# Optimization experiments

Measured on AMD Instinct MI355X. Metric: run time of the kernel, lower is better.

Reference implementation:

```python
import jax, jax.numpy as jnp
import numpy as np

LS = (0, 1, 2)
DIMS = tuple(2 * l + 1 for l in LS)          # (1, 3, 5)
MULS = (128, 64, 32)                          # node irreps multiplicities (= attention*heads)
ATT_MULS = (16, 8, 4)                         # attention_irreps multiplicities per head
N_HEADS = 8
N_IRREPS_ATT = sum(ATT_MULS)                  # 28
ATTN_NORM = 1.0 / np.sqrt(N_IRREPS_ATT)
CG = tuple(1.0 / np.sqrt(d) for d in DIMS)    # l (x) l -> 0e Clebsch-Gordan coefficient
N_NODES = 512
EDGE_ATTR_DIM = 32
NODE_DIM = sum(m * d for m, d in zip(MULS, DIMS))  # 480


def split_irreps(x, muls):
    """Split last axis into per-l blocks [..., mul_l, 2l+1]."""
    out, i = [], 0
    for mul, d in zip(muls, DIMS):
        out.append(x[..., i:i + mul * d].reshape(x.shape[:-1] + (mul, d)))
        i += mul * d
    return out


def merge_irreps(parts):
    return jnp.concatenate([p.reshape(p.shape[:-2] + (-1,)) for p in parts], axis=-1)


def e3_linear(parts, Ws):
    # equivariant linear: mixes multiplicities within each l, 1/sqrt(mul_in) norm
    return [jnp.einsum('nim,io->nom', p, W) / np.sqrt(p.shape[-2])
            for p, W in zip(parts, Ws)]


def setup_inputs() -> dict:
    key = jax.random.key(0)
    ks = jax.random.split(key, 16)
    inp = {
        'node_feat': jax.random.normal(ks[0], (N_NODES, NODE_DIM), jnp.float32),
        'edge_attr': jax.random.normal(ks[1], (N_NODES, N_NODES, EDGE_ATTR_DIM), jnp.float32),
        'edge_sh':   jax.random.normal(ks[2], (N_NODES, N_NODES, sum(DIMS)), jnp.float32),
    }
    i = 3
    for nm in ('Wq', 'Wk', 'Wv'):
        for l, mul in enumerate(MULS):
            inp[f'{nm}{l}'] = jax.random.normal(ks[i], (mul, mul), jnp.float32)
            i += 1
    inp['mW1'] = jax.random.normal(ks[i], (EDGE_ATTR_DIM + 2 * sum(MULS), 64), jnp.float32) * 0.05
    inp['mb1'] = jnp.zeros((64,), jnp.float32)
    inp['mW2'] = jax.random.normal(ks[i + 1], (64, 64), jnp.float32) * 0.1
    inp['mb2'] = jnp.zeros((64,), jnp.float32)
    inp['mW3'] = jax.random.normal(ks[i + 2], (64, N_HEADS), jnp.float32) * 0.1
    inp['mb3'] = jnp.zeros((N_HEADS,), jnp.float32)
    return inp


def reference(node_feat, edge_attr, edge_sh,
              Wq0, Wq1, Wq2, Wk0, Wk1, Wk2, Wv0, Wv1, Wv2,
              mW1, mb1, mW2, mb2, mW3, mb3):
    N = node_feat.shape[0]
    nf = split_irreps(node_feat, MULS)                 # per-l: [N, mul_l, 2l+1]
    sh = split_irreps(edge_sh, (1, 1, 1))              # per-l: [N, N, 1, 2l+1]

    def to_heads(parts):
        return [p.reshape(N, N_HEADS, am, d) for p, am, d in zip(parts, ATT_MULS, DIMS)]

    q = to_heads(e3_linear(nf, (Wq0, Wq1, Wq2)))
    k = to_heads(e3_linear(nf, (Wk0, Wk1, Wk2)))
    v = to_heads(e3_linear(nf, (Wv0, Wv1, Wv2)))

    # node (x) edge_sh -> scalars (0e): same-l inner products, CG = 1/sqrt(2l+1)
    feat_rec = jnp.concatenate(
        [jnp.einsum('rim,rsm->rsi', p, s[..., 0, :]) * c for p, s, c in zip(nf, sh, CG)], axis=-1)
    feat_snd = jnp.concatenate(
        [jnp.einsum('sim,rsm->rsi', p, s[..., 0, :]) * c for p, s, c in zip(nf, sh, CG)], axis=-1)
    edge_feat = jnp.concatenate([edge_attr, feat_rec, feat_snd], axis=-1)  # [N,N,480]

    h = jnp.tanh(edge_feat @ mW1 + mb1)
    h = jnp.tanh(h @ mW2 + mb2)
    edge_weight = h @ mW3 + mb3                        # [N, N, H]

    # elementwise q (x) k -> 0e, summed over irreps (== scaled dot product per head)
    logits = sum(jnp.einsum('rhim,shim->rsh', qp, kp) * c
                 for qp, kp, c in zip(q, k, CG))       # [N, N, H]
    weight = jax.nn.softmax(logits * ATTN_NORM + edge_weight, axis=-2)  # softmax over senders

    # weighted aggregation over senders, per irrep
    upd = [jnp.einsum('rsh,shim->rhim', weight, vp) for vp in v]
    # axis_to_mul: [N, H, mul, d] -> [N, H*mul, d]
    upd = [u.reshape(N, N_HEADS * am, d) for u, am, d in zip(upd, ATT_MULS, DIMS)]

    return node_feat + merge_irreps(upd)               # residual (irreps match)
```

## Files before the change

kernel.cpp:

```cpp
#include <hip/hip_runtime.h>
#include <hip/hip_bf16.h>
#include <stdint.h>


#define NNODES 512
#define NDIM   480

#define QG_OFF    0u
#define W2B_OFF   131072u
#define W3B_OFF   133120u
#define KG_OFF    245760u
#define VB_OFF    491520u
#define ARE_OFF   737280u
#define ASN_OFF   884736u
#define WF_OFF    1032192u
#define FLAG_OFF  1040384u
#define L_OFF     1040448u
#define WTQ_OFF   3137600u
#define WTK_OFF   3159104u
#define WTV_OFF   3180608u
#define W1T_OFF   3202112u

typedef float f32x4 __attribute__((ext_vector_type(4)));
typedef short s16x8 __attribute__((ext_vector_type(8)));

__device__ __forceinline__ float bf2f(uint16_t u) {
    return __uint_as_float(((uint32_t)u) << 16);
}
__device__ __forceinline__ uint16_t f2bf(float f) {
    union { __hip_bfloat16 h; uint16_t u; } cv;
    cv.h = __float2bfloat16(f);
    return cv.u;
}
__device__ __forceinline__ uint32_t packbf(float lo, float hi) {
    return ((uint32_t)f2bf(hi) << 16) | (uint32_t)f2bf(lo);
}
__device__ __forceinline__ float ldin(const void* p, size_t i, int f32) {
    return f32 ? ((const float*)p)[i] : bf2f(((const uint16_t*)p)[i]);
}
__device__ __forceinline__ float ftanh(float x) {
    float e = __builtin_amdgcn_exp2f(x * 2.885390081777927f);
    return 1.0f - 2.0f * __builtin_amdgcn_rcpf(e + 1.0f);
}

#define NS 16384
__global__ __launch_bounds__(256) void kW(
    const void* __restrict__ mW1, const void* __restrict__ mb1,
    const void* __restrict__ mW2, const void* __restrict__ mb2,
    const void* __restrict__ mW3, const void* __restrict__ mb3,
    const void* __restrict__ Wq0, const void* __restrict__ Wq1, const void* __restrict__ Wq2,
    const void* __restrict__ Wk0, const void* __restrict__ Wk1, const void* __restrict__ Wk2,
    const void* __restrict__ Wv0, const void* __restrict__ Wv1, const void* __restrict__ Wv2,
    float* __restrict__ ws, const void* __restrict__ nfu, int* __restrict__ flagp)
{
    __shared__ int sflag;
    const int t = threadIdx.x;
    if (t < 64) {
        uint32_t x = ((const uint32_t*)nfu)[64 + t];
        int e = (x >> 7) & 0xff;
        int good = (x != 0u) && (e >= 100) && (e <= 140);
        unsigned long long m = __ballot(good);
        if (t == 0) sflag = (__popcll(m) < 32) ? 1 : 0;
    }
    __syncthreads();
    const int f32 = sflag;
    if (blockIdx.x == 0 && t == 0) flagp[0] = f32;

    const int gt = blockIdx.x * 256 + t;
    float* Wf = ws + WF_OFF;

    for (int i = gt; i < 2048; i += NS) Wf[i] = ldin(mW1, i, f32);
    for (int i = gt; i < 64; i += NS) Wf[6656 + i] = ldin(mb1, i, f32);
    for (int i = gt; i < 64; i += NS) Wf[6720 + i] = ldin(mb2, i, f32);
    for (int i = gt; i < 8; i += NS)  Wf[6784 + i] = ldin(mb3, i, f32);

    {
        uint32_t* W2B = (uint32_t*)(ws + W2B_OFF);
        for (int i = gt; i < 2048; i += NS) {
            int f = i >> 8, lane = (i >> 2) & 63, w = i & 3;
            int nt = f >> 1, ks = f & 1, nl2 = lane & 15, gg = lane >> 4;
            int n = nt * 16 + nl2, kb = ks * 32 + gg * 8 + 2 * w;
            float lo = ldin(mW2, (size_t)kb * 64 + n, f32);
            float hi = ldin(mW2, (size_t)(kb + 1) * 64 + n, f32);
            W2B[i] = packbf(lo, hi);
        }
        uint32_t* W3B = (uint32_t*)(ws + W3B_OFF);
        for (int i = gt; i < 512; i += NS) {
            int ks = i >> 8, lane = (i >> 2) & 63, w = i & 3;
            int nl2 = lane & 15, gg = lane >> 4;
            int kb = ks * 32 + gg * 8 + 2 * w;
            float lo = (nl2 < 8) ? ldin(mW3, (size_t)kb * 8 + nl2, f32) : 0.f;
            float hi = (nl2 < 8) ? ldin(mW3, (size_t)(kb + 1) * 8 + nl2, f32) : 0.f;
            W3B[i] = packbf(lo, hi);
        }
    }

    const float e3n0 = 0.08838834764831845f, e3n1 = 0.125f, e3n2 = 0.17677669529663687f;
    const float cg1 = 0.5773502691896258f, cg2 = 0.4472135954999579f;
    const float attn = 0.1889822365046136f;

    const void* Wsrc[9] = {Wq0, Wq1, Wq2, Wk0, Wk1, Wk2, Wv0, Wv1, Wv2};
    float* Wdst[3] = {ws + WTQ_OFF, ws + WTK_OFF, ws + WTV_OFF};
    for (int kind = 0; kind < 3; ++kind) {
        const float f0 = (kind == 0) ? e3n0 * attn : e3n0;
        const float f1 = (kind == 0) ? e3n1 * cg1 * attn : e3n1;
        const float f2 = (kind == 0) ? e3n2 * cg2 * attn : e3n2;
        for (int i = gt; i < 16384; i += NS) {
            int o = i >> 7, ii = i & 127;
            Wdst[kind][i] = ldin(Wsrc[kind * 3], (size_t)ii * 128 + o, f32) * f0;
        }
        for (int i = gt; i < 4096; i += NS) {
            int o = i >> 6, ii = i & 63;
            Wdst[kind][16384 + i] = ldin(Wsrc[kind * 3 + 1], (size_t)ii * 64 + o, f32) * f1;
        }
        for (int i = gt; i < 1024; i += NS) {
            int o = i >> 5, ii = i & 31;
            Wdst[kind][20480 + i] = ldin(Wsrc[kind * 3 + 2], (size_t)ii * 32 + o, f32) * f2;
        }
    }
    float* W1T = ws + W1T_OFF;
    for (int i = gt; i < 30720; i += NS) {
        int o = i / 480, row = i - o * 480;
        float cgv;
        if (row < 160)      cgv = 1.0f;
        else if (row < 224) cgv = cg1;
        else if (row < 256) cgv = cg2;
        else if (row < 384) cgv = 1.0f;
        else if (row < 448) cgv = cg1;
        else                cgv = cg2;
        W1T[i] = ldin(mW1, (size_t)row * 64 + o, f32) * cgv;
    }
}

__global__ __launch_bounds__(256) void kA(
    const void* __restrict__ nfu,
    const float* __restrict__ WtQ, const float* __restrict__ WtK,
    const float* __restrict__ WtV, const float* __restrict__ W1T,
    uint32_t* __restrict__ qG, uint32_t* __restrict__ kG, float* __restrict__ vB,
    uint32_t* __restrict__ ArecG, uint32_t* __restrict__ AsndG,
    const int* __restrict__ flagp)
{
    const int f32 = flagp[0];
    const int n = blockIdx.x, t = threadIdx.x;
    __shared__ float nfs[480];
    for (int i = t; i < 480; i += 256) nfs[i] = ldin(nfu, (size_t)n * 480 + i, f32);

    if (t < 64) {
        const int kind2 = t >> 5, hh = (t >> 2) & 7, j = 60 + (t & 3);
        const int row = n & 15, rt = n >> 4;
        const int cc = (j >> 3) ^ (n & 7);
        uint16_t* dst = (uint16_t*)(kind2 == 0 ? qG : kG);
        dst[((((size_t)rt * 8 + hh) * 16 + row) * 8 + cc) * 8 + (j & 7)] = 0;
    }
    __syncthreads();

    for (int idx = t; idx < 1440; idx += 256) {
        int kind = idx / 480, rem = idx - kind * 480;
        int o, m, mul, d, off, am, qoff, sub;
        if (rem < 128)      { o = rem;           m = 0;          mul = 128; d = 1; off = 0;   am = 16; qoff = 0;  sub = 0; }
        else if (rem < 320) { int x = rem - 128; o = x / 3; m = x - o * 3; mul = 64;  d = 3; off = 128; am = 8;  qoff = 16; sub = 16384; }
        else                { int x = rem - 320; o = x / 5; m = x - o * 5; mul = 32;  d = 5; off = 320; am = 4;  qoff = 40; sub = 20480; }
        const float* base = (kind == 0) ? WtQ : (kind == 1) ? WtK : WtV;
        const float4* W4 = reinterpret_cast<const float4*>(base + sub + o * mul);
        const float* nf0 = nfs + off + m;
        float ax = 0.f, ay = 0.f, az = 0.f, aw = 0.f;
        const int n4 = mul >> 2;
        for (int i4 = 0; i4 < n4; ++i4) {
            float4 w = W4[i4];
            int ib = 4 * i4 * d;
            ax += nf0[ib]         * w.x;
            ay += nf0[ib + d]     * w.y;
            az += nf0[ib + 2 * d] * w.z;
            aw += nf0[ib + 3 * d] * w.w;
        }
        float acc = (ax + ay) + (az + aw);
        if (kind == 2) {
            vB[(size_t)n * 480 + rem] = acc;
        } else {
            int hh = o / am, a = o - hh * am;
            int j = qoff + a * d + m;
            const int row = n & 15, rt = n >> 4;
            const int cc = (j >> 3) ^ (n & 7);
            uint16_t* dst = (uint16_t*)(kind == 0 ? qG : kG);
            dst[((((size_t)rt * 8 + hh) * 16 + row) * 8 + cc) * 8 + (j & 7)] = f2bf(acc);
        }
    }

    if (t < 128) {
        const int src = t >> 6, o = t & 63;
        float a[9];
        #pragma unroll
        for (int mi = 0; mi < 9; ++mi) {
            const int l = (mi == 0) ? 0 : (mi < 4 ? 1 : 2);
            const int m = (mi == 0) ? 0 : (mi < 4 ? mi - 1 : mi - 4);
            const int mul = (l == 0 ? 128 : l == 1 ? 64 : 32);
            const int d = 2 * l + 1;
            const int off = (l == 0 ? 0 : l == 1 ? 128 : 320);
            const int base = (src == 0) ? (l == 0 ? 32 : l == 1 ? 160 : 224)
                                        : (l == 0 ? 256 : l == 1 ? 384 : 448);
            const float4* W4 = reinterpret_cast<const float4*>(W1T + o * 480 + base);
            const float* nf0 = nfs + off + m;
            float ax = 0.f, ay = 0.f, az = 0.f, aw = 0.f;
            const int n4 = mul >> 2;
            for (int i4 = 0; i4 < n4; ++i4) {
                float4 w = W4[i4];
                int ib = 4 * i4 * d;
                ax += nf0[ib]         * w.x;
                ay += nf0[ib + d]     * w.y;
                az += nf0[ib + 2 * d] * w.z;
                aw += nf0[ib + 3 * d] * w.w;
            }
            a[mi] = (ax + ay) + (az + aw);
        }
        float b[9];
        #pragma unroll
        for (int mi = 0; mi < 9; ++mi) b[mi] = __shfl_xor(a[mi], 1, 64);
        if ((o & 1) == 0) {
            uint32_t* dst = (src ? AsndG : ArecG) + (size_t)n * 288 + (o >> 1);
            #pragma unroll
            for (int mi = 0; mi < 9; ++mi)
                dst[mi * 32] = ((uint32_t)f2bf(b[mi]) << 16) | (uint32_t)f2bf(a[mi]);
        }
    }
}

__global__ __launch_bounds__(256, 4) void kB(
    const void* __restrict__ eaG, const void* __restrict__ shG,
    const uint32_t* __restrict__ ArecG, const uint32_t* __restrict__ AsndG,
    const uint32_t* __restrict__ qG, const uint32_t* __restrict__ kG,
    const uint32_t* __restrict__ W2B, const uint32_t* __restrict__ W3B,
    const float* __restrict__ Wf, float* __restrict__ L,
    const int* __restrict__ flagp)
{
    __shared__ __align__(16) uint32_t smem[10240];
    uint32_t* ArecS = smem;
    uint32_t* AsndS = smem + 4672;
    float* ewS = (float*)(smem + 8192);
    const int f32 = flagp[0];
    const int t = threadIdx.x;
    const int s0 = blockIdx.x * 16, r0 = blockIdx.y * 16;
    const int lane = t & 63, wv = t >> 6;
    const int g = lane >> 4, nl = lane & 15;

    const int rl = t >> 4, sl = t & 15;
    const int r = r0 + rl, s = s0 + sl;
    const size_t eidx = (((size_t)r) << 9) + s;

    uint32_t eaR[16];
    if (f32) {
        const float4* ep = reinterpret_cast<const float4*>((const float*)eaG + eidx * 32);
        #pragma unroll
        for (int i = 0; i < 8; ++i) {
            float4 v = ep[i];
            eaR[2 * i]     = ((uint32_t)f2bf(v.y) << 16) | (uint32_t)f2bf(v.x);
            eaR[2 * i + 1] = ((uint32_t)f2bf(v.w) << 16) | (uint32_t)f2bf(v.z);
        }
    } else {
        const uint4* ep = reinterpret_cast<const uint4*>((const uint32_t*)eaG + eidx * 16);
        #pragma unroll
        for (int i = 0; i < 4; ++i) {
            uint4 v = ep[i];
            eaR[4 * i] = v.x; eaR[4 * i + 1] = v.y; eaR[4 * i + 2] = v.z; eaR[4 * i + 3] = v.w;
        }
    }

    float sh0, sh1, sh2, sh3, sh4, sh5, sh6, sh7, sh8;
    {
        const size_t sb = eidx * 9;
        if (f32) {
            const float* shp = (const float*)shG + sb;
            sh0 = shp[0]; sh1 = shp[1]; sh2 = shp[2]; sh3 = shp[3]; sh4 = shp[4];
            sh5 = shp[5]; sh6 = shp[6]; sh7 = shp[7]; sh8 = shp[8];
        } else {
            const uint16_t* shp = (const uint16_t*)shG + sb;
            sh0 = bf2f(shp[0]); sh1 = bf2f(shp[1]); sh2 = bf2f(shp[2]);
            sh3 = bf2f(shp[3]); sh4 = bf2f(shp[4]); sh5 = bf2f(shp[5]);
            sh6 = bf2f(shp[6]); sh7 = bf2f(shp[7]); sh8 = bf2f(shp[8]);
        }
    }

    for (int i = t; i < 16 * 288; i += 256) {
        int row = i / 288, c = i - row * 288;
        ArecS[row * 292 + c] = ArecG[(size_t)(r0 + row) * 288 + c];
        AsndS[row * 292 + c] = AsndG[(size_t)(s0 + row) * 288 + c];
    }

    float h[64];
    #pragma unroll
    for (int o = 0; o < 64; ++o) h[o] = Wf[6656 + o];

    __syncthreads();

    {
        const int rb = rl * 292, sb = sl * 292;
        #pragma unroll 1
        for (int mi = 0; mi < 9; ++mi) {
            float shv = sh0;
            shv = (mi == 1) ? sh1 : shv;  shv = (mi == 2) ? sh2 : shv;
            shv = (mi == 3) ? sh3 : shv;  shv = (mi == 4) ? sh4 : shv;
            shv = (mi == 5) ? sh5 : shv;  shv = (mi == 6) ? sh6 : shv;
            shv = (mi == 7) ? sh7 : shv;  shv = (mi == 8) ? sh8 : shv;
            const int ro = rb + mi * 32, so = sb + mi * 32;
            #pragma unroll
            for (int oc = 0; oc < 32; ++oc) {
                uint32_t pa = ArecS[ro + oc];
                uint32_t pb = AsndS[so + oc];
                float a0 = __uint_as_float(pa << 16);
                float b0 = __uint_as_float(pb << 16);
                float a1 = __uint_as_float(pa & 0xffff0000u);
                float b1 = __uint_as_float(pb & 0xffff0000u);
                h[2 * oc]     += shv * (a0 + b0);
                h[2 * oc + 1] += shv * (a1 + b1);
            }
        }
    }

    {
        #pragma unroll 1
        for (int cd = 0; cd < 16; ++cd) {
            uint32_t p = eaR[cd];
            float e0 = __uint_as_float(p << 16);
            float e1 = __uint_as_float(p & 0xffff0000u);
            const float* w0 = Wf + (2 * cd) * 64;
            #pragma unroll
            for (int o = 0; o < 64; ++o) h[o] += e0 * w0[o];
            #pragma unroll
            for (int o = 0; o < 64; ++o) h[o] += e1 * w0[64 + o];
        }
    }

    #pragma unroll
    for (int o = 0; o < 64; ++o) h[o] = ftanh(h[o]);

    __syncthreads();
    #pragma unroll
    for (int c = 0; c < 8; ++c) {
        const int cc = c ^ (t & 7);
        *(uint4*)&smem[t * 32 + cc * 4] =
            make_uint4(packbf(h[c * 8 + 0], h[c * 8 + 1]),
                       packbf(h[c * 8 + 2], h[c * 8 + 3]),
                       packbf(h[c * 8 + 4], h[c * 8 + 5]),
                       packbf(h[c * 8 + 6], h[c * 8 + 7]));
    }
    __builtin_amdgcn_sched_barrier(0);

    s16x8 w2f[4][2];
    #pragma unroll
    for (int nt = 0; nt < 4; ++nt) {
        #pragma unroll
        for (int ks = 0; ks < 2; ++ks)
            w2f[nt][ks] = ((const s16x8*)W2B)[(nt * 2 + ks) * 64 + lane];
    }
    s16x8 w3f[2];
    w3f[0] = ((const s16x8*)W3B)[lane];
    w3f[1] = ((const s16x8*)W3B)[64 + lane];
    float b2v[4];
    #pragma unroll
    for (int nt = 0; nt < 4; ++nt) b2v[nt] = Wf[6720 + nt * 16 + nl];
    const float b3v = (nl < 8) ? Wf[6784 + nl] : 0.f;


    uint16_t* sm16 = (uint16_t*)smem;
    #pragma unroll 1
    for (int mm = 0; mm < 4; ++mm) {
        const int mt = wv * 4 + mm;
        const int row = mt * 16 + nl;
        const int sw0 = ((g    ) ^ (row & 7)) * 4;
        const int sw1 = ((4 + g) ^ (row & 7)) * 4;
        const s16x8 a0 = *(const s16x8*)&smem[row * 32 + sw0];
        const s16x8 a1 = *(const s16x8*)&smem[row * 32 + sw1];
        f32x4 acc[4];
        #pragma unroll
        for (int nt = 0; nt < 4; ++nt) {
            f32x4 a = {b2v[nt], b2v[nt], b2v[nt], b2v[nt]};
            a = __builtin_amdgcn_mfma_f32_16x16x32_bf16(a0, w2f[nt][0], a, 0, 0, 0);
            a = __builtin_amdgcn_mfma_f32_16x16x32_bf16(a1, w2f[nt][1], a, 0, 0, 0);
            acc[nt] = a;
        }
        const int e2base = mt * 16 + g * 4;
        #pragma unroll
        for (int nt = 0; nt < 4; ++nt) {
            const int n = nt * 16 + nl;
            #pragma unroll
            for (int rg = 0; rg < 4; ++rg) {
                const int e2 = e2base + rg;
                const int cc = (n >> 3) ^ (e2 & 7);
                sm16[e2 * 64 + cc * 8 + (n & 7)] = f2bf(ftanh(acc[nt][rg]));
            }
        }
        const s16x8 c0 = *(const s16x8*)&smem[row * 32 + sw0];
        const s16x8 c1 = *(const s16x8*)&smem[row * 32 + sw1];
        f32x4 a3 = {b3v, b3v, b3v, b3v};
        a3 = __builtin_amdgcn_mfma_f32_16x16x32_bf16(c0, w3f[0], a3, 0, 0, 0);
        a3 = __builtin_amdgcn_mfma_f32_16x16x32_bf16(c1, w3f[1], a3, 0, 0, 0);
        if (nl < 8) {
            #pragma unroll
            for (int rg = 0; rg < 4; ++rg) {
                const int e2 = mt * 16 + g * 4 + rg;
                ewS[nl * 256 + (e2 ^ (nl << 2))] = a3[rg];
            }
        }
    }

    __syncthreads();

    {
        const uint4* qg4 = (const uint4*)qG + (size_t)blockIdx.y * 1024;
        const uint4* kg4 = (const uint4*)kG + (size_t)blockIdx.x * 1024;
        uint4* sm4 = (uint4*)smem;
        for (int i = t; i < 2048; i += 256)
            sm4[i] = (i < 1024) ? qg4[i] : kg4[i - 1024];
    }
    __syncthreads();

    {
        const int sw0 = ((g    ) ^ (nl & 7)) << 2;
        const int sw1 = ((4 + g) ^ (nl & 7)) << 2;
        #pragma unroll
        for (int hh2 = 0; hh2 < 2; ++hh2) {
            const int h = wv * 2 + hh2;
            const uint32_t* qb = smem + h * 512;
            const uint32_t* kb = smem + 4096 + h * 512;
            const s16x8 qa0 = *(const s16x8*)&qb[nl * 32 + sw0];
            const s16x8 qa1 = *(const s16x8*)&qb[nl * 32 + sw1];
            const s16x8 ka0 = *(const s16x8*)&kb[nl * 32 + sw0];
            const s16x8 ka1 = *(const s16x8*)&kb[nl * 32 + sw1];
            f32x4 a = {0.f, 0.f, 0.f, 0.f};
            a = __builtin_amdgcn_mfma_f32_16x16x32_bf16(qa0, ka0, a, 0, 0, 0);
            a = __builtin_amdgcn_mfma_f32_16x16x32_bf16(qa1, ka1, a, 0, 0, 0);
            float* Lp = L + (((size_t)h) << 18) + (((size_t)(r0 + g * 4)) << 9) + s0 + nl;
            #pragma unroll
            for (int rg = 0; rg < 4; ++rg) {
                const int e2 = (g * 4 + rg) * 16 + nl;
                Lp[(size_t)rg << 9] = a[rg] + ewS[h * 256 + (e2 ^ (h << 2))];
            }
        }
    }
}

__global__ __launch_bounds__(512) void kAgg(
    const float* __restrict__ L, const float* __restrict__ vB,
    const void* __restrict__ nfu, void* __restrict__ out,
    const int* __restrict__ flagp)
{
    __shared__ float Ls[8192];
    const int f32 = flagp[0];
    const int t = threadIdx.x;
    const int r0 = blockIdx.x * 2;

    {
        const int grp = t >> 5, l = t & 31;
        const int rr = grp >> 3, hsm = grp & 7;
        const float* Lg = L + (((size_t)hsm) << 18) + (((size_t)(r0 + rr)) << 9);
        float v[16];
        float mx = -3.402823466e38f;
        #pragma unroll
        for (int i = 0; i < 16; ++i) {
            v[i] = Lg[l + 32 * i];
            mx = fmaxf(mx, v[i]);
        }
        #pragma unroll
        for (int off = 16; off >= 1; off >>= 1) mx = fmaxf(mx, __shfl_xor(mx, off, 32));
        const float C = 1.4426950408889634f;
        float sm = 0.f;
        #pragma unroll
        for (int i = 0; i < 16; ++i) {
            v[i] = __builtin_amdgcn_exp2f((v[i] - mx) * C);
            sm += v[i];
        }
        #pragma unroll
        for (int off = 16; off >= 1; off >>= 1) sm += __shfl_xor(sm, off, 32);
        const float inv = __builtin_amdgcn_rcpf(sm);
        #pragma unroll
        for (int i = 0; i < 16; ++i)
            Ls[rr * 4096 + (l + 32 * i) * 8 + hsm] = v[i] * inv;
    }
    __syncthreads();

    if (t >= 240) return;
    const int j0 = 2 * t;
    int hh;
    if (j0 < 128)      hh = j0 >> 4;
    else if (j0 < 320) hh = (j0 - 128) / 24;
    else               hh = (j0 - 320) / 20;

    const float* L0 = Ls + hh;
    const float* L1 = Ls + 4096 + hh;
    float a0 = 0.f, a1 = 0.f, b0 = 0.f, b1 = 0.f;
    const float2* vp = reinterpret_cast<const float2*>(vB + j0);
    #pragma unroll 8
    for (int s = 0; s < 512; ++s) {
        float2 v = vp[(size_t)s * 240];
        float w0 = L0[s * 8], w1 = L1[s * 8];
        a0 += w0 * v.x; a1 += w0 * v.y;
        b0 += w1 * v.x; b1 += w1 * v.y;
    }

    const size_t o0 = (size_t)r0 * 480 + j0;
    const size_t o1 = o0 + 480;
    float r00 = ldin(nfu, o0, f32) + a0;
    float r01 = ldin(nfu, o0 + 1, f32) + a1;
    float r10 = ldin(nfu, o1, f32) + b0;
    float r11 = ldin(nfu, o1 + 1, f32) + b1;
    if (f32) {
        float* op = (float*)out;
        op[o0] = r00; op[o0 + 1] = r01;
        op[o1] = r10; op[o1 + 1] = r11;
    } else {
        uint16_t* op = (uint16_t*)out;
        op[o0] = f2bf(r00); op[o0 + 1] = f2bf(r01);
        op[o1] = f2bf(r10); op[o1 + 1] = f2bf(r11);
    }
}

extern "C" void kernel_launch(void* const* d_in, const int* in_sizes, int n_in,
                              void* d_out, int out_size, void* d_ws, size_t ws_size,
                              hipStream_t stream)
{
    (void)in_sizes; (void)n_in; (void)out_size; (void)ws_size;
    const void* nf  = d_in[0];
    const void* eaG = d_in[1];
    const void* shG = d_in[2];

    float* ws = (float*)d_ws;
    uint32_t* qG = (uint32_t*)(ws + QG_OFF);
    uint32_t* kG = (uint32_t*)(ws + KG_OFF);
    uint32_t* W2B = (uint32_t*)(ws + W2B_OFF);
    uint32_t* W3B = (uint32_t*)(ws + W3B_OFF);
    float* vB  = ws + VB_OFF;
    uint32_t* ArecG = (uint32_t*)(ws + ARE_OFF);
    uint32_t* AsndG = (uint32_t*)(ws + ASN_OFF);
    float* Wf  = ws + WF_OFF;
    int* flag  = (int*)(ws + FLAG_OFF);
    float* L   = ws + L_OFF;
    float* WtQ = ws + WTQ_OFF;
    float* WtK = ws + WTK_OFF;
    float* WtV = ws + WTV_OFF;
    float* W1T = ws + W1T_OFF;

    kW<<<64, 256, 0, stream>>>(d_in[12], d_in[13], d_in[14], d_in[15], d_in[16], d_in[17],
                               d_in[3], d_in[4], d_in[5], d_in[6], d_in[7], d_in[8],
                               d_in[9], d_in[10], d_in[11], ws, nf, flag);
    kA<<<512, 256, 0, stream>>>(nf, WtQ, WtK, WtV, W1T, qG, kG, vB, ArecG, AsndG, flag);
    kB<<<dim3(32, 32), 256, 0, stream>>>(eaG, shG, ArecG, AsndG, qG, kG, W2B, W3B, Wf, L, flag);
    kAgg<<<256, 512, 0, stream>>>(L, vB, nf, d_out, flag);
}
```

Measured before the change: 222.0 us.

## Compute attention aggregation with bf16 MFMA using transposed per-head V layout

The aggregation kernel now performs the weighted sum over senders as a bf16 16x16x32 MFMA matmul, replacing scalar FMA loops. kA writes V transposed per head as bf16, padded to 64 columns. The softmax weights are packed to bf16 in swizzled shared memory, and the grid becomes 32x8 blocks (16 rows by one head). This cuts the scalar work and the strided fp32 V reads, but rounds the weights and V to bf16, which reduces accuracy.

```diff
diff --git a/kernel.cpp b/kernel.cpp
--- a/kernel.cpp
+++ b/kernel.cpp
@@ -10,7 +10,7 @@
 #define W2B_OFF   131072u
 #define W3B_OFF   133120u
 #define KG_OFF    245760u
-#define VB_OFF    491520u
+#define VT_OFF    491520u
 #define ARE_OFF   737280u
 #define ASN_OFF   884736u
 #define WF_OFF    1032192u
@@ -136,7 +136,7 @@
     const void* __restrict__ nfu,
     const float* __restrict__ WtQ, const float* __restrict__ WtK,
     const float* __restrict__ WtV, const float* __restrict__ W1T,
-    uint32_t* __restrict__ qG, uint32_t* __restrict__ kG, float* __restrict__ vB,
+    uint32_t* __restrict__ qG, uint32_t* __restrict__ kG, uint16_t* __restrict__ vT,
     uint32_t* __restrict__ ArecG, uint32_t* __restrict__ AsndG,
     const int* __restrict__ flagp)
 {
@@ -145,12 +145,16 @@
     __shared__ float nfs[480];
     for (int i = t; i < 480; i += 256) nfs[i] = ldin(nfu, (size_t)n * 480 + i, f32);
 
-    if (t < 64) {
-        const int kind2 = t >> 5, hh = (t >> 2) & 7, j = 60 + (t & 3);
-        const int row = n & 15, rt = n >> 4;
-        const int cc = (j >> 3) ^ (n & 7);
-        uint16_t* dst = (uint16_t*)(kind2 == 0 ? qG : kG);
-        dst[((((size_t)rt * 8 + hh) * 16 + row) * 8 + cc) * 8 + (j & 7)] = 0;
+    if (t < 96) {
+        const int kind3 = t >> 5, hh = (t >> 2) & 7, j = 60 + (t & 3);
+        if (kind3 < 2) {
+            const int row = n & 15, rt = n >> 4;
+            const int cc = (j >> 3) ^ (n & 7);
+            uint16_t* dst = (uint16_t*)(kind3 == 0 ? qG : kG);
+            dst[((((size_t)rt * 8 + hh) * 16 + row) * 8 + cc) * 8 + (j & 7)] = 0;
+        } else {
+            vT[((size_t)(hh * 64 + j)) * 512 + n] = 0;
+        }
     }
     __syncthreads();
 
@@ -174,11 +178,11 @@
             aw += nf0[ib + 3 * d] * w.w;
         }
         float acc = (ax + ay) + (az + aw);
+        int hh = o / am, a = o - hh * am;
+        int j = qoff + a * d + m;
         if (kind == 2) {
-            vB[(size_t)n * 480 + rem] = acc;
+            vT[((size_t)(hh * 64 + j)) * 512 + n] = f2bf(acc);
         } else {
-            int hh = o / am, a = o - hh * am;
-            int j = qoff + a * d + m;
             const int row = n & 15, rt = n >> 4;
             const int cc = (j >> 3) ^ (n & 7);
             uint16_t* dst = (uint16_t*)(kind == 0 ? qG : kG);
@@ -438,78 +442,81 @@
     }
 }
 
-__global__ __launch_bounds__(512) void kAgg(
-    const float* __restrict__ L, const float* __restrict__ vB,
+__global__ __launch_bounds__(256) void kAgg(
+    const float* __restrict__ L, const uint16_t* __restrict__ vT,
     const void* __restrict__ nfu, void* __restrict__ out,
     const int* __restrict__ flagp)
 {
-    __shared__ float Ls[8192];
+    __shared__ __align__(16) uint32_t Ws[4096];
     const int f32 = flagp[0];
     const int t = threadIdx.x;
-    const int r0 = blockIdx.x * 2;
-
-    {
-        const int grp = t >> 5, l = t & 31;
-        const int rr = grp >> 3, hsm = grp & 7;
-        const float* Lg = L + (((size_t)hsm) << 18) + (((size_t)(r0 + rr)) << 9);
-        float v[16];
+    const int lane = t & 63, wv = t >> 6;
+    const int g = lane >> 4, nl = lane & 15;
+    const int r0 = blockIdx.x * 16;
+    const int h  = blockIdx.y;
+
+    {
+        const int row = wv * 4 + g;
+        const float* Lg = L + (((size_t)h) << 18) + (((size_t)(r0 + row)) << 9);
+        float v[32];
+        #pragma unroll
+        for (int cw = 0; cw < 4; ++cw) {
+            const float4* p = reinterpret_cast<const float4*>(Lg + nl * 8 + cw * 128);
+            float4 x = p[0], y = p[1];
+            v[cw * 8 + 0] = x.x; v[cw * 8 + 1] = x.y; v[cw * 8 + 2] = x.z; v[cw * 8 + 3] = x.w;
+            v[cw * 8 + 4] = y.x; v[cw * 8 + 5] = y.y; v[cw * 8 + 6] = y.z; v[cw * 8 + 7] = y.w;
+        }
         float mx = -3.402823466e38f;
         #pragma unroll
-        for (int i = 0; i < 16; ++i) {
-            v[i] = Lg[l + 32 * i];
-            mx = fmaxf(mx, v[i]);
-        }
-        #pragma unroll
-        for (int off = 16; off >= 1; off >>= 1) mx = fmaxf(mx, __shfl_xor(mx, off, 32));
+        for (int i = 0; i < 32; ++i) mx = fmaxf(mx, v[i]);
+        #pragma unroll
+        for (int off = 8; off >= 1; off >>= 1) mx = fmaxf(mx, __shfl_xor(mx, off, 16));
         const float C = 1.4426950408889634f;
         float sm = 0.f;
         #pragma unroll
-        for (int i = 0; i < 16; ++i) {
+        for (int i = 0; i < 32; ++i) {
             v[i] = __builtin_amdgcn_exp2f((v[i] - mx) * C);
             sm += v[i];
         }
         #pragma unroll
-        for (int off = 16; off >= 1; off >>= 1) sm += __shfl_xor(sm, off, 32);
+        for (int off = 8; off >= 1; off >>= 1) sm += __shfl_xor(sm, off, 16);
         const float inv = __builtin_amdgcn_rcpf(sm);
         #pragma unroll
-        for (int i = 0; i < 16; ++i)
-            Ls[rr * 4096 + (l + 32 * i) * 8 + hsm] = v[i] * inv;
-    }
-    __syncthreads();
-
-    if (t >= 240) return;
-    const int j0 = 2 * t;
-    int hh;
-    if (j0 < 128)      hh = j0 >> 4;
-    else if (j0 < 320) hh = (j0 - 128) / 24;
-    else               hh = (j0 - 320) / 20;
-
-    const float* L0 = Ls + hh;
-    const float* L1 = Ls + 4096 + hh;
-    float a0 = 0.f, a1 = 0.f, b0 = 0.f, b1 = 0.f;
-    const float2* vp = reinterpret_cast<const float2*>(vB + j0);
-    #pragma unroll 8
-    for (int s = 0; s < 512; ++s) {
-        float2 v = vp[(size_t)s * 240];
-        float w0 = L0[s * 8], w1 = L1[s * 8];
-        a0 += w0 * v.x; a1 += w0 * v.y;
-        b0 += w1 * v.x; b1 += w1 * v.y;
-    }
-
-    const size_t o0 = (size_t)r0 * 480 + j0;
-    const size_t o1 = o0 + 480;
-    float r00 = ldin(nfu, o0, f32) + a0;
-    float r01 = ldin(nfu, o0 + 1, f32) + a1;
-    float r10 = ldin(nfu, o1, f32) + b0;
-    float r11 = ldin(nfu, o1 + 1, f32) + b1;
-    if (f32) {
-        float* op = (float*)out;
-        op[o0] = r00; op[o0 + 1] = r01;
-        op[o1] = r10; op[o1 + 1] = r11;
-    } else {
-        uint16_t* op = (uint16_t*)out;
-        op[o0] = f2bf(r00); op[o0 + 1] = f2bf(r01);
-        op[o1] = f2bf(r10); op[o1 + 1] = f2bf(r11);
+        for (int cw = 0; cw < 4; ++cw) {
+            const int cc = (nl + cw * 16) ^ (row & 7);
+            *(uint4*)&Ws[row * 256 + cc * 4] = make_uint4(
+                packbf(v[cw * 8 + 0] * inv, v[cw * 8 + 1] * inv),
+                packbf(v[cw * 8 + 2] * inv, v[cw * 8 + 3] * inv),
+                packbf(v[cw * 8 + 4] * inv, v[cw * 8 + 5] * inv),
+                packbf(v[cw * 8 + 6] * inv, v[cw * 8 + 7] * inv));
+        }
+    }
+    __syncthreads();
+
+    f32x4 acc = {0.f, 0.f, 0.f, 0.f};
+    {
+        const uint16_t* vb = vT + ((size_t)(h * 64 + wv * 16 + nl)) * 512 + g * 8;
+        #pragma unroll
+        for (int ks = 0; ks < 16; ++ks) {
+            const s16x8 a = *(const s16x8*)&Ws[nl * 256 + (((ks * 4 + g) ^ (nl & 7)) << 2)];
+            const s16x8 b = *(const s16x8*)&vb[ks * 32];
+            acc = __builtin_amdgcn_mfma_f32_16x16x32_bf16(a, b, acc, 0, 0, 0);
+        }
+    }
+
+    const int n = wv * 16 + nl;
+    if (n < 60) {
+        int col;
+        if (n < 16)      col = h * 16 + n;
+        else if (n < 40) col = 128 + h * 24 + (n - 16);
+        else             col = 320 + h * 20 + (n - 40);
+        #pragma unroll
+        for (int rg = 0; rg < 4; ++rg) {
+            const size_t o = (size_t)(r0 + g * 4 + rg) * 480 + col;
+            float val = ldin(nfu, o, f32) + acc[rg];
+            if (f32) ((float*)out)[o] = val;
+            else     ((uint16_t*)out)[o] = f2bf(val);
+        }
     }
 }
 
@@ -527,7 +534,7 @@
     uint32_t* kG = (uint32_t*)(ws + KG_OFF);
     uint32_t* W2B = (uint32_t*)(ws + W2B_OFF);
     uint32_t* W3B = (uint32_t*)(ws + W3B_OFF);
-    float* vB  = ws + VB_OFF;
+    uint16_t* vT = (uint16_t*)(ws + VT_OFF);
     uint32_t* ArecG = (uint32_t*)(ws + ARE_OFF);
     uint32_t* AsndG = (uint32_t*)(ws + ASN_OFF);
     float* Wf  = ws + WF_OFF;
@@ -541,7 +548,7 @@
     kW<<<64, 256, 0, stream>>>(d_in[12], d_in[13], d_in[14], d_in[15], d_in[16], d_in[17],
                                d_in[3], d_in[4], d_in[5], d_in[6], d_in[7], d_in[8],
                                d_in[9], d_in[10], d_in[11], ws, nf, flag);
-    kA<<<512, 256, 0, stream>>>(nf, WtQ, WtK, WtV, W1T, qG, kG, vB, ArecG, AsndG, flag);
+    kA<<<512, 256, 0, stream>>>(nf, WtQ, WtK, WtV, W1T, qG, kG, vT, ArecG, AsndG, flag);
     kB<<<dim3(32, 32), 256, 0, stream>>>(eaG, shG, ArecG, AsndG, qG, kG, W2B, W3B, Wf, L, flag);
-    kAgg<<<256, 512, 0, stream>>>(L, vB, nf, d_out, flag);
-}
+    kAgg<<<dim3(32, 8), 256, 0, stream>>>(L, vT, nf, d_out, flag);
+}
```

New measurement: 198.6 us. 10.5% less time.
